# Kernel optimization log

Hardware: AMD Instinct MI355X
Metric: run time of the kernel (lower is better)

Reference implementation:

```python
import jax, jax.numpy as jnp
import numpy as np

N, K, IN, OUT, H = 20000, 32, 128, 256, 64  # H = OUT // 4 (bottleneck hidden)
EPS = 1e-5

def leaky(x):
    return jnp.where(x >= 0, x, 0.1 * x)

def bn(x, g, b, axes):
    # training-mode batch norm: batch statistics over `axes`, per-channel affine
    m = jnp.mean(x, axis=axes, keepdims=True)
    v = jnp.var(x, axis=axes, keepdims=True)
    return (x - m) * jax.lax.rsqrt(v + EPS) * g + b

def setup_inputs() -> dict:
    key = jax.random.key(0)
    ks = jax.random.split(key, 12)
    q_pts = jax.random.normal(ks[0], (N, 3), jnp.float32)
    return {
        'features': jax.random.normal(ks[1], (N, IN), jnp.float32),
        'q_pts': q_pts,
        's_pts': q_pts,  # non-strided block: queries == supports
        'neighb_inds': jax.random.randint(ks[2], (N, K), 0, N, dtype=jnp.int32),
        'w_unary1': jax.random.normal(ks[3], (IN, H), jnp.float32) * 0.05,
        'g1': jnp.ones(H, jnp.float32), 'b1': jnp.zeros(H, jnp.float32),
        'w_conv0': jax.random.normal(ks[4], (H, H), jnp.float32) * 0.05,
        'g_bn0': jnp.ones(H, jnp.float32), 'b_bn0': jnp.zeros(H, jnp.float32),
        'w_conv1': jax.random.normal(ks[5], (H, H * 3), jnp.float32) * 0.05,
        'g_bn1': jnp.ones(H, jnp.float32), 'b_bn1': jnp.zeros(H, jnp.float32),
        'g_bnc': jnp.ones(H, jnp.float32), 'b_bnc': jnp.zeros(H, jnp.float32),
        'w_unary2': jax.random.normal(ks[6], (H, OUT), jnp.float32) * 0.05,
        'g2': jnp.ones(OUT, jnp.float32), 'b2': jnp.zeros(OUT, jnp.float32),
        'w_sc': jax.random.normal(ks[7], (IN, OUT), jnp.float32) * 0.05,
        'g_sc': jnp.ones(OUT, jnp.float32), 'b_sc': jnp.zeros(OUT, jnp.float32),
    }

def reference(features, q_pts, s_pts, neighb_inds,
              w_unary1, g1, b1,
              w_conv0, g_bn0, b_bn0,
              w_conv1, g_bn1, b_bn1,
              g_bnc, b_bnc,
              w_unary2, g2, b2,
              w_sc, g_sc, b_sc):
    # unary1: Linear -> BN1d -> LeakyReLU
    x = leaky(bn(features @ w_unary1, g1, b1, 0))              # [N, H]
    # pad with zero shadow row (index N = out-of-range neighbor)
    s_pad = jnp.concatenate([s_pts, jnp.zeros((1, 3), s_pts.dtype)], 0)
    f_pad = jnp.concatenate([x, jnp.zeros((1, H), x.dtype)], 0)
    nb_x = s_pad[neighb_inds] - q_pts[:, None, :]              # [N, K, 3]
    nb_y = f_pad[neighb_inds]                                  # [N, K, H]
    # adaptive kernel generation: 1x1 conv -> BN2d -> LeakyReLU -> 1x1 conv
    k0 = leaky(bn(jnp.einsum('nkc,cd->nkd', nb_y, w_conv0), g_bn0, b_bn0, (0, 1)))
    kern = jnp.einsum('nkd,de->nke', k0, w_conv1).reshape(N, K, H, 3)
    # per-neighbor dynamic matmul: [H,3] @ [3] per (n,k)
    msg = jnp.einsum('nkhc,nkc->nkh', kern, nb_x)              # [N, K, H]
    msg = leaky(bn(msg, g_bn1, b_bn1, (0, 1)))
    agg = jnp.max(msg, axis=1)                                 # [N, H] max over neighbors
    # batch_norm_conv + LeakyReLU
    agg = leaky(bn(agg, g_bnc, b_bnc, 0))
    # unary2 (no relu) + shortcut (no relu)
    xo = bn(agg @ w_unary2, g2, b2, 0)                         # [N, OUT]
    sc = bn(features @ w_sc, g_sc, b_sc, 0)                    # [N, OUT]
    return leaky(xo + sc)
```

## Files before the change

kernel.cpp:

```cpp
#include <hip/hip_runtime.h>

#define KNB 32
#define CIN 128
#define CH 64
#define COUT 256
#define BN_EPS 1e-5f
#define CONV_GRID 256

typedef __attribute__((ext_vector_type(8))) short bf16x8;
typedef __attribute__((ext_vector_type(4))) float f32x4;

static __device__ __forceinline__ float leakyf(float v){ return fmaxf(v, 0.1f*v); }

static __device__ __forceinline__ unsigned short f2bf(float f){
    unsigned u = __float_as_uint(f);
    u += 0x7FFFu + ((u >> 16) & 1u);
    return (unsigned short)(u >> 16);
}
static __device__ __forceinline__ float bf2f(ushort u){ return __uint_as_float(((unsigned)u) << 16); }

static __device__ __forceinline__ unsigned cvtpk(float lo, float hi){
    unsigned r;
    asm("v_cvt_pk_bf16_f32 %0, %1, %2" : "=v"(r) : "v"(lo), "v"(hi));
    return r;
}

static __device__ __forceinline__ void bn_affine_wave(const float* __restrict__ G, const float* __restrict__ s,
    const float* __restrict__ W, const float* __restrict__ gg, const float* __restrict__ bb,
    float invcnt, int D, int M, int o, int lane, float& ai, float& ci)
{
    float pm = 0.f, pq = 0.f;
    for (int j = lane; j < D; j += 64){
        float wj = W[j*M + o];
        pm += s[j]*wj;
        float t = 0.f;
        for (int i = 0; i < D; ++i) t += G[i*D + j]*W[i*M + o];
        pq += wj*t;
    }
    #pragma unroll
    for (int off = 32; off; off >>= 1){
        pm += __shfl_down(pm, off);
        pq += __shfl_down(pq, off);
    }
    float m  = pm*invcnt;
    float var = pq*invcnt - m*m;
    float a_ = gg[o]*rsqrtf(var + BN_EPS);
    float c_ = bb[o] - m*a_;
    ai = __shfl(a_, 0);
    ci = __shfl(c_, 0);
}

__global__ __launch_bounds__(512) void k1_kernel(const float* __restrict__ feat, const int* __restrict__ inds,
    const float* __restrict__ W1, int N,
    float* __restrict__ slabA, ushort* __restrict__ featbf, ushort* __restrict__ w1s,
    ushort* __restrict__ xbf, float* __restrict__ cnt)
{
    __shared__ ushort Xt[128][40];
    __shared__ float red[16][128];
    int tid = threadIdx.x, bid = blockIdx.x;
    if (bid < 128){
        int wave = tid >> 6, lane = tid & 63, l15 = lane & 15, g = lane >> 4;
        int wr = wave >> 1, wc = wave & 1;
        const f32x4 z4 = {0.f,0.f,0.f,0.f};
        f32x4 acc[2][4];
        #pragma unroll
        for (int i=0;i<2;++i)
            #pragma unroll
            for (int j=0;j<4;++j) acc[i][j] = z4;
        float pcs[4] = {0,0,0,0};
        int nch = (N + 31) >> 5;
        for (int ch = bid; ch < nch; ch += 128){
            int base = ch << 5;
            __syncthreads();
            #pragma unroll
            for (int ii=0; ii<2; ++ii){
                int i = tid + ii*512;
                int r = i >> 5, c4 = i & 31;
                int n = base + r;
                float4 v = make_float4(0.f,0.f,0.f,0.f);
                if (n < N) v = ((const float4*)feat)[(size_t)n*32 + c4];
                ushort b0=f2bf(v.x), b1=f2bf(v.y), b2=f2bf(v.z), b3=f2bf(v.w);
                Xt[c4*4+0][r]=b0; Xt[c4*4+1][r]=b1; Xt[c4*4+2][r]=b2; Xt[c4*4+3][r]=b3;
                pcs[0]+=bf2f(b0); pcs[1]+=bf2f(b1); pcs[2]+=bf2f(b2); pcs[3]+=bf2f(b3);
            }
            __syncthreads();
            bf16x8 af[2], bv[4];
            #pragma unroll
            for (int t=0;t<2;++t) af[t] = *(const bf16x8*)&Xt[wr*32 + t*16 + l15][g*8];
            #pragma unroll
            for (int u=0;u<4;++u) bv[u] = *(const bf16x8*)&Xt[wc*64 + u*16 + l15][g*8];
            #pragma unroll
            for (int t=0;t<2;++t)
                #pragma unroll
                for (int u=0;u<4;++u)
                    acc[t][u] = __builtin_amdgcn_mfma_f32_16x16x32_bf16(af[t], bv[u], acc[t][u], 0,0,0);
        }
        float* Gp = slabA + (size_t)bid*16512;
        #pragma unroll
        for (int t=0;t<2;++t)
            #pragma unroll
            for (int u=0;u<4;++u)
                #pragma unroll
                for (int q=0;q<4;++q)
                    Gp[(wr*32 + t*16 + g*4 + q)*CIN + wc*64 + u*16 + l15] = acc[t][u][q];
        __syncthreads();
        { int r16 = tid >> 5, c4 = tid & 31;
          #pragma unroll
          for (int j=0;j<4;++j) red[r16][c4*4+j] = pcs[j]; }
        __syncthreads();
        if (tid < CIN){
            float s = 0.f;
            #pragma unroll
            for (int k=0;k<16;++k) s += red[k][tid];
            Gp[16384 + tid] = s;
        }
    } else {
        int t2 = (bid-128)*512 + tid;
        const int TG = 128*512;
        for (int i = t2; i < N*32; i += TG){
            float4 v = ((const float4*)feat)[i];
            uint2 pk; pk.x = cvtpk(v.x, v.y); pk.y = cvtpk(v.z, v.w);
            ((uint2*)featbf)[i] = pk;
        }
        for (int i = t2; i < N*KNB; i += TG){
            int ix = inds[i];
            if ((unsigned)ix < (unsigned)N) atomicAdd(&cnt[ix], 1.0f);
        }
        if (t2 < 192*CH){
            int r = t2 >> 6, dd = t2 & 63;
            int c = r >> 6, h = r & 63;
            w1s[t2] = f2bf(W1[dd*192 + 3*h + c]);
        }
        if (t2 < CH) xbf[(size_t)N*CH + t2] = 0;
    }
}

__global__ __launch_bounds__(256) void reduce_slab(const float* __restrict__ slab, int nparts, int len,
                                                   float* __restrict__ dst)
{
    int j = blockIdx.x*256 + threadIdx.x;
    if (j < len){
        float s0 = 0.f, s1 = 0.f, s2 = 0.f, s3 = 0.f;
        int b = 0;
        for (; b + 4 <= nparts; b += 4){
            s0 += slab[(size_t)(b+0)*len + j];
            s1 += slab[(size_t)(b+1)*len + j];
            s2 += slab[(size_t)(b+2)*len + j];
            s3 += slab[(size_t)(b+3)*len + j];
        }
        for (; b < nparts; ++b) s0 += slab[(size_t)b*len + j];
        dst[j] = (s0 + s1) + (s2 + s3);
    }
}

__global__ __launch_bounds__(512) void k3_finA(const float* __restrict__ XtX, const float* __restrict__ fsum,
    const float* __restrict__ Wu1, const float* __restrict__ g1, const float* __restrict__ b1,
    const float* __restrict__ Wsc, const float* __restrict__ gsc, const float* __restrict__ bsc,
    float invN, float* __restrict__ c1v, ushort* __restrict__ w1t,
    ushort* __restrict__ wcat, float* __restrict__ cscv)
{
    int gw = blockIdx.x*8 + (threadIdx.x >> 6), lane = threadIdx.x & 63;
    if (gw < 64){
        int o = gw; float ai, ci;
        bn_affine_wave(XtX, fsum, Wu1, g1, b1, invN, CIN, CH, o, lane, ai, ci);
        if (lane == 0) c1v[o] = ci;
        for (int k = lane; k < CIN; k += 64) w1t[o*CIN + k] = f2bf(ai*Wu1[k*CH + o]);
    } else if (gw < 320){
        int o = gw - 64; float ai, ci;
        bn_affine_wave(XtX, fsum, Wsc, gsc, bsc, invN, CIN, COUT, o, lane, ai, ci);
        if (lane == 0) cscv[o] = ci;
        for (int k = lane; k < CIN; k += 64) wcat[o*192 + k] = f2bf(ai*Wsc[k*COUT + o]);
    }
}

__global__ __launch_bounds__(512) void k4_unary1_gram(const ushort* __restrict__ featbf,
    const ushort* __restrict__ w1t, const float* __restrict__ c1v, const float* __restrict__ cnt,
    ushort* __restrict__ xbf, float* __restrict__ slabB, int N)
{
    __shared__ ushort Xp[64][136];
    __shared__ ushort Xw[64][136];
    __shared__ float red[8][64];
    int tid = threadIdx.x, bid = blockIdx.x;
    int wave = tid >> 6, lane = tid & 63, l15 = lane & 15, g = lane >> 4;
    const f32x4 z4 = {0.f,0.f,0.f,0.f};
    int row0 = bid*128 + wave*16;
    f32x4 acc[4] = {z4, z4, z4, z4};
    int r = row0 + l15;
    bool ok = r < N;
    #pragma unroll
    for (int s=0;s<4;++s){
        bf16x8 af = {0,0,0,0,0,0,0,0};
        if (ok) af = *(const bf16x8*)(featbf + (size_t)r*CIN + s*32 + g*8);
        #pragma unroll
        for (int nt=0;nt<4;++nt){
            bf16x8 bfr = *(const bf16x8*)(w1t + (size_t)(nt*16+l15)*CIN + s*32 + g*8);
            acc[nt] = __builtin_amdgcn_mfma_f32_16x16x32_bf16(af, bfr, acc[nt], 0,0,0);
        }
    }
    float wq[4];
    #pragma unroll
    for (int q=0;q<4;++q){
        int rr = row0 + g*4 + q;
        wq[q] = (rr < N) ? cnt[rr] : 0.f;
    }
    float ps[4] = {0,0,0,0};
    #pragma unroll
    for (int nt=0;nt<4;++nt){
        int col = nt*16 + l15;
        float cc = c1v[col];
        #pragma unroll
        for (int q=0;q<4;++q){
            int rr = row0 + g*4 + q;
            int lr = wave*16 + g*4 + q;
            float v = (rr < N) ? leakyf(acc[nt][q] + cc) : 0.f;
            ushort b = f2bf(v);
            if (rr < N) xbf[(size_t)rr*CH + col] = b;
            Xp[col][lr] = b;
            float wv = wq[q]*v;
            Xw[col][lr] = f2bf(wv);
            ps[nt] += wv;
        }
    }
    #pragma unroll
    for (int nt=0;nt<4;++nt){
        ps[nt] += __shfl_xor(ps[nt], 16);
        ps[nt] += __shfl_xor(ps[nt], 32);
        if (lane < 16) red[wave][nt*16 + l15] = ps[nt];
    }
    __syncthreads();
    int mr = wave >> 1, ncb = (wave & 1)*2;
    f32x4 ac2[2] = {z4, z4};
    #pragma unroll
    for (int ks=0;ks<4;++ks){
        bf16x8 af = *(const bf16x8*)&Xw[mr*16 + l15][ks*32 + g*8];
        #pragma unroll
        for (int u=0;u<2;++u){
            bf16x8 bv = *(const bf16x8*)&Xp[(ncb+u)*16 + l15][ks*32 + g*8];
            ac2[u] = __builtin_amdgcn_mfma_f32_16x16x32_bf16(af, bv, ac2[u], 0,0,0);
        }
    }
    float* Gp = slabB + (size_t)bid*4160;
    #pragma unroll
    for (int u=0;u<2;++u)
        #pragma unroll
        for (int q=0;q<4;++q)
            Gp[(mr*16 + g*4 + q)*CH + (ncb+u)*16 + l15] = ac2[u][q];
    if (tid < CH){
        float s = 0.f;
        #pragma unroll
        for (int w8=0;w8<8;++w8) s += red[w8][tid];
        Gp[4096 + tid] = s;
    }
}

__global__ __launch_bounds__(512) void k5_fin0(const float* __restrict__ G0, const float* __restrict__ s0,
    const float* __restrict__ W0, const float* __restrict__ gb0, const float* __restrict__ bb0,
    float invNK, float* __restrict__ c0p, ushort* __restrict__ w0t)
{
    int gw = blockIdx.x*8 + (threadIdx.x >> 6), lane = threadIdx.x & 63;
    if (gw < 64){
        float ai, ci;
        bn_affine_wave(G0, s0, W0, gb0, bb0, invNK, CH, CH, gw, lane, ai, ci);
        if (lane == 0) c0p[gw] = ci;
        w0t[gw*CH + lane] = f2bf(ai*W0[lane*CH + gw]);
    }
}

__global__ __launch_bounds__(512) void conv_msg_mfma(
    const ushort* __restrict__ xbf, const float* __restrict__ qp, const float* __restrict__ sp,
    const int* __restrict__ inds, const ushort* __restrict__ w0t, const ushort* __restrict__ w1s,
    const float* __restrict__ c0p,
    float* __restrict__ mx, float* __restrict__ mn, float* __restrict__ msgpart, int N)
{
    __shared__ unsigned char SM[24576 + 8*12288];
    int tid = threadIdx.x, bid = blockIdx.x;
    int warp = tid >> 6, lane = tid & 63;
    int l15 = lane & 15, g = lane >> 4;
    for (int ch = tid; ch < 1536; ch += 512){
        int r = ch >> 3, c16 = ch & 7;
        uint4 v = ((const uint4*)w1s)[ch];
        *(uint4*)(SM + r*128 + ((c16*16) ^ ((r&7)<<4))) = v;
    }
    bf16x8 wf[8];
    #pragma unroll
    for (int mt=0;mt<4;++mt)
        #pragma unroll
        for (int s=0;s<2;++s)
            wf[mt*2+s] = *(const bf16x8*)(w0t + (mt*16+l15)*CH + s*32 + g*8);
    float c0r[16];
    #pragma unroll
    for (int mt=0;mt<4;++mt)
        #pragma unroll
        for (int q=0;q<4;++q)
            c0r[mt*4+q] = c0p[mt*16 + g*4 + q];
    unsigned char* k0base = SM + 24576 + warp*12288;
    unsigned swz = (unsigned)((l15 & 7) << 4);
    float ps[4] = {0,0,0,0}, pss[4] = {0,0,0,0};
    const f32x4 z4 = {0.f,0.f,0.f,0.f};
    __syncthreads();

    for (int n = bid*8 + warp; n < N; n += CONV_GRID*8){
        int ix0 = inds[n*KNB + l15];
        int ix1 = inds[n*KNB + 16 + l15];
        if ((unsigned)ix0 > (unsigned)N) ix0 = N;
        if ((unsigned)ix1 > (unsigned)N) ix1 = N;
        float qx = qp[n*3+0], qy = qp[n*3+1], qz = qp[n*3+2];
        float nbv[2][3];
        if (ix0 < N){ nbv[0][0]=sp[ix0*3]-qx; nbv[0][1]=sp[ix0*3+1]-qy; nbv[0][2]=sp[ix0*3+2]-qz; }
        else        { nbv[0][0]=-qx; nbv[0][1]=-qy; nbv[0][2]=-qz; }
        if (ix1 < N){ nbv[1][0]=sp[ix1*3]-qx; nbv[1][1]=sp[ix1*3+1]-qy; nbv[1][2]=sp[ix1*3+2]-qz; }
        else        { nbv[1][0]=-qx; nbv[1][1]=-qy; nbv[1][2]=-qz; }
        bf16x8 xf0a = *(const bf16x8*)(xbf + (size_t)ix0*CH +      g*8);
        bf16x8 xf0b = *(const bf16x8*)(xbf + (size_t)ix0*CH + 32 + g*8);
        bf16x8 xf1a = *(const bf16x8*)(xbf + (size_t)ix1*CH +      g*8);
        bf16x8 xf1b = *(const bf16x8*)(xbf + (size_t)ix1*CH + 32 + g*8);
        f32x4 acc0[8];
        #pragma unroll
        for (int i=0;i<8;++i) acc0[i] = z4;
        #pragma unroll
        for (int mt=0;mt<4;++mt){
            acc0[mt*2+0] = __builtin_amdgcn_mfma_f32_16x16x32_bf16(wf[mt*2+0], xf0a, acc0[mt*2+0], 0,0,0);
            acc0[mt*2+0] = __builtin_amdgcn_mfma_f32_16x16x32_bf16(wf[mt*2+1], xf0b, acc0[mt*2+0], 0,0,0);
            acc0[mt*2+1] = __builtin_amdgcn_mfma_f32_16x16x32_bf16(wf[mt*2+0], xf1a, acc0[mt*2+1], 0,0,0);
            acc0[mt*2+1] = __builtin_amdgcn_mfma_f32_16x16x32_bf16(wf[mt*2+1], xf1b, acc0[mt*2+1], 0,0,0);
        }
        #pragma unroll
        for (int mt=0;mt<4;++mt){
            #pragma unroll
            for (int ntk=0;ntk<2;++ntk){
                f32x4 a = acc0[mt*2+ntk];
                float v0 = leakyf(a[0] + c0r[mt*4+0]);
                float v1 = leakyf(a[1] + c0r[mt*4+1]);
                float v2 = leakyf(a[2] + c0r[mt*4+2]);
                float v3 = leakyf(a[3] + c0r[mt*4+3]);
                #pragma unroll
                for (int c=0;c<3;++c){
                    float w = nbv[ntk][c];
                    uint2 pk;
                    pk.x = cvtpk(v0*w, v1*w);
                    pk.y = cvtpk(v2*w, v3*w);
                    *(uint2*)(k0base + (c*32 + ntk*16 + l15)*128 + ((unsigned)(mt*32 + g*8) ^ swz)) = pk;
                }
            }
        }
        f32x4 acc1[8];
        #pragma unroll
        for (int i=0;i<8;++i) acc1[i] = z4;
        #pragma unroll
        for (int c=0;c<3;++c){
            #pragma unroll
            for (int ks=0;ks<2;++ks){
                unsigned co = ((unsigned)(ks*64 + g*16)) ^ swz;
                bf16x8 a0f = *(const bf16x8*)(k0base + (c*32 +      l15)*128 + co);
                bf16x8 a1f = *(const bf16x8*)(k0base + (c*32 + 16 + l15)*128 + co);
                #pragma unroll
                for (int nt=0;nt<4;++nt){
                    bf16x8 bfr = *(const bf16x8*)(SM + (c*64 + nt*16 + l15)*128 + co);
                    acc1[0*4+nt] = __builtin_amdgcn_mfma_f32_16x16x32_bf16(a0f, bfr, acc1[0*4+nt], 0,0,0);
                    acc1[1*4+nt] = __builtin_amdgcn_mfma_f32_16x16x32_bf16(a1f, bfr, acc1[1*4+nt], 0,0,0);
                }
            }
        }
        #pragma unroll
        for (int nt=0;nt<4;++nt){
            float vmx = -3.4e38f, vmn = 3.4e38f, s = 0.f, ssq = 0.f;
            #pragma unroll
            for (int mtk=0;mtk<2;++mtk){
                f32x4 a = acc1[mtk*4+nt];
                #pragma unroll
                for (int q=0;q<4;++q){
                    float v = a[q];
                    vmx = fmaxf(vmx, v); vmn = fminf(vmn, v);
                    s += v; ssq += v*v;
                }
            }
            vmx = fmaxf(vmx, __shfl_xor(vmx, 16)); vmn = fminf(vmn, __shfl_xor(vmn, 16));
            s  += __shfl_xor(s, 16);               ssq += __shfl_xor(ssq, 16);
            vmx = fmaxf(vmx, __shfl_xor(vmx, 32)); vmn = fminf(vmn, __shfl_xor(vmn, 32));
            s  += __shfl_xor(s, 32);               ssq += __shfl_xor(ssq, 32);
            if (lane < 16){
                mx[(size_t)n*CH + nt*16 + l15] = vmx;
                mn[(size_t)n*CH + nt*16 + l15] = vmn;
                ps[nt] += s; pss[nt] += ssq;
            }
        }
    }
    __syncthreads();
    float* red = (float*)SM;
    if (lane < 16){
        #pragma unroll
        for (int nt=0;nt<4;++nt){
            red[warp*128 + nt*16 + l15]        = ps[nt];
            red[1024 + warp*128 + nt*16 + l15] = pss[nt];
        }
    }
    __syncthreads();
    if (tid < 64){
        float s = 0.f, ssq = 0.f;
        #pragma unroll
        for (int w8=0;w8<8;++w8){ s += red[w8*128 + tid]; ssq += red[1024 + w8*128 + tid]; }
        msgpart[(size_t)bid*128 + tid]      = s;
        msgpart[(size_t)bid*128 + 64 + tid] = ssq;
    }
}

__global__ __launch_bounds__(512) void k7_agg(const float* __restrict__ mxb, const float* __restrict__ mnb,
    const float* __restrict__ msgpart, const float* __restrict__ gb1, const float* __restrict__ bb1,
    float* __restrict__ aggb, float* __restrict__ aggpart, int N)
{
    __shared__ float r1[512], r2[512];
    __shared__ float a1ms[64], c1ms[64];
    int tid = threadIdx.x, bid = blockIdx.x;
    {
        int t = tid & 63, seg = tid >> 6;
        float s = 0.f, ss = 0.f;
        for (int r = seg; r < CONV_GRID; r += 8){ s += msgpart[r*128 + t]; ss += msgpart[r*128 + 64 + t]; }
        r1[tid] = s; r2[tid] = ss;
    }
    __syncthreads();
    if (tid < 64){
        float S = 0.f, SS = 0.f;
        #pragma unroll
        for (int k=0;k<8;++k){ S += r1[tid + 64*k]; SS += r2[tid + 64*k]; }
        float invc = 1.0f/((float)N*KNB);
        float m = S*invc, var = SS*invc - m*m;
        float ai = gb1[tid]*rsqrtf(var + BN_EPS);
        a1ms[tid] = ai; c1ms[tid] = bb1[tid] - m*ai;
    }
    __syncthreads();
    int h = tid & 63;
    float ah = a1ms[h], chh = c1ms[h];
    bool useMax = (ah >= 0.f);
    float ps = 0.f, pss = 0.f;
    for (int i = bid*512 + tid; i < N*CH; i += gridDim.x*512){
        float sel = useMax ? mxb[i] : mnb[i];
        float v = leakyf(ah*sel + chh);
        aggb[i] = v; ps += v; pss += v*v;
    }
    __syncthreads();
    r1[tid] = ps; r2[tid] = pss;
    __syncthreads();
    if (tid < 64){
        float S = 0.f, SS = 0.f;
        #pragma unroll
        for (int k=0;k<8;++k){ S += r1[tid + 64*k]; SS += r2[tid + 64*k]; }
        aggpart[(size_t)bid*128 + tid]      = S;
        aggpart[(size_t)bid*128 + 64 + tid] = SS;
    }
}

__global__ __launch_bounds__(512) void k8_gram64t(const float* __restrict__ aggb, const float* __restrict__ aggpart,
    const float* __restrict__ gbc, const float* __restrict__ bbc,
    ushort* __restrict__ a2b2, float* __restrict__ slabC, int N)
{
    __shared__ ushort Xt[64][72];
    __shared__ float red[32][64];
    __shared__ float abncs[64], cbncs[64];
    int tid = threadIdx.x, bid = blockIdx.x;
    int wave = tid >> 6, lane = tid & 63, l15 = lane & 15, g = lane >> 4;
    const f32x4 z4 = {0.f,0.f,0.f,0.f};
    {
        float* r1 = &red[0][0]; float* r2 = r1 + 512;
        int t = tid & 63, seg = tid >> 6;
        float s = 0.f, ss = 0.f;
        for (int r = seg; r < 256; r += 8){ s += aggpart[r*128 + t]; ss += aggpart[r*128 + 64 + t]; }
        r1[tid] = s; r2[tid] = ss;
        __syncthreads();
        if (tid < 64){
            float S = 0.f, SS = 0.f;
            #pragma unroll
            for (int k=0;k<8;++k){ S += r1[tid + 64*k]; SS += r2[tid + 64*k]; }
            float invc = 1.0f/(float)N;
            float m = S*invc, var = SS*invc - m*m;
            float ai = gbc[tid]*rsqrtf(var + BN_EPS);
            abncs[tid] = ai; cbncs[tid] = bbc[tid] - m*ai;
        }
        __syncthreads();
    }
    int wr = wave >> 1, wc = wave & 1;
    f32x4 acc[2] = {z4, z4};
    float pcs[4] = {0,0,0,0};
    int nch = (N + 63) >> 6;
    for (int ch = bid; ch < nch; ch += 256){
        int base = ch << 6;
        __syncthreads();
        #pragma unroll
        for (int ii=0;ii<2;++ii){
            int i = tid + ii*512;
            int r = i >> 4, cq = i & 15;
            int n = base + r;
            float4 v = make_float4(0.f,0.f,0.f,0.f);
            if (n < N){
                v = ((const float4*)aggb)[(size_t)n*16 + cq];
                v.x = leakyf(abncs[cq*4+0]*v.x + cbncs[cq*4+0]);
                v.y = leakyf(abncs[cq*4+1]*v.y + cbncs[cq*4+1]);
                v.z = leakyf(abncs[cq*4+2]*v.z + cbncs[cq*4+2]);
                v.w = leakyf(abncs[cq*4+3]*v.w + cbncs[cq*4+3]);
            }
            uint2 pk; pk.x = cvtpk(v.x, v.y); pk.y = cvtpk(v.z, v.w);
            if (n < N) ((uint2*)a2b2)[(size_t)n*16 + cq] = pk;
            Xt[cq*4+0][r] = (ushort)(pk.x & 0xffff);
            Xt[cq*4+1][r] = (ushort)(pk.x >> 16);
            Xt[cq*4+2][r] = (ushort)(pk.y & 0xffff);
            Xt[cq*4+3][r] = (ushort)(pk.y >> 16);
            pcs[0] += v.x; pcs[1] += v.y; pcs[2] += v.z; pcs[3] += v.w;
        }
        __syncthreads();
        #pragma unroll
        for (int ks=0;ks<2;++ks){
            bf16x8 af = *(const bf16x8*)&Xt[wr*16 + l15][ks*32 + g*8];
            #pragma unroll
            for (int u=0;u<2;++u){
                bf16x8 bv = *(const bf16x8*)&Xt[wc*32 + u*16 + l15][ks*32 + g*8];
                acc[u] = __builtin_amdgcn_mfma_f32_16x16x32_bf16(af, bv, acc[u], 0,0,0);
            }
        }
    }
    float* Gp = slabC + (size_t)bid*4160;
    #pragma unroll
    for (int u=0;u<2;++u)
        #pragma unroll
        for (int q=0;q<4;++q)
            Gp[(wr*16 + g*4 + q)*CH + wc*32 + u*16 + l15] = acc[u][q];
    __syncthreads();
    { int r = tid >> 4, cq = tid & 15;
      #pragma unroll
      for (int j=0;j<4;++j) red[r][cq*4+j] = pcs[j]; }
    __syncthreads();
    if (tid < CH){
        float s = 0.f;
        #pragma unroll
        for (int k=0;k<32;++k) s += red[k][tid];
        Gp[4096 + tid] = s;
    }
}

__global__ __launch_bounds__(512) void k10_fin2(const float* __restrict__ G2, const float* __restrict__ s2,
    const float* __restrict__ Wu2, const float* __restrict__ g2, const float* __restrict__ b2,
    const float* __restrict__ cscv, float invN, ushort* __restrict__ wcat, float* __restrict__ ccomb)
{
    int gw = blockIdx.x*8 + (threadIdx.x >> 6), lane = threadIdx.x & 63;
    if (gw < 256){
        float ai, ci;
        bn_affine_wave(G2, s2, Wu2, g2, b2, invN, CH, COUT, gw, lane, ai, ci);
        wcat[gw*192 + 128 + lane] = f2bf(ai*Wu2[lane*COUT + gw]);
        if (lane == 0) ccomb[gw] = cscv[gw] + ci;
    }
}

__global__ __launch_bounds__(512) void final_mfma_kernel(
    const ushort* __restrict__ featbf, const ushort* __restrict__ a2b2,
    const ushort* __restrict__ wcat, const float* __restrict__ ccomb,
    float* __restrict__ out, int N)
{
    int tid = threadIdx.x, wave = tid >> 6, lane = tid & 63;
    int l15 = lane & 15, g = lane >> 4;
    int row0 = blockIdx.x*128 + wave*16;
    const f32x4 z4 = {0.f,0.f,0.f,0.f};
    f32x4 acc[16];
    #pragma unroll
    for (int i=0;i<16;++i) acc[i] = z4;
    int r = row0 + l15;
    bool ok = r < N;
    #pragma unroll
    for (int s=0;s<6;++s){
        bf16x8 af = {0,0,0,0,0,0,0,0};
        if (ok){
            const ushort* srcp = (s < 4) ? (featbf + (size_t)r*CIN + s*32 + g*8)
                                         : (a2b2  + (size_t)r*CH + (s-4)*32 + g*8);
            af = *(const bf16x8*)srcp;
        }
        #pragma unroll
        for (int nt=0;nt<16;++nt){
            bf16x8 bfr = *(const bf16x8*)(wcat + (nt*16+l15)*192 + s*32 + g*8);
            acc[nt] = __builtin_amdgcn_mfma_f32_16x16x32_bf16(af, bfr, acc[nt], 0,0,0);
        }
    }
    #pragma unroll
    for (int nt=0;nt<16;++nt){
        float cc = ccomb[nt*16 + l15];
        #pragma unroll
        for (int q=0;q<4;++q){
            int rr = row0 + g*4 + q;
            if (rr < N) out[(size_t)rr*COUT + nt*16 + l15] = leakyf(acc[nt][q] + cc);
        }
    }
}

extern "C" void kernel_launch(void* const* d_in, const int* in_sizes, int n_in,
                              void* d_out, int out_size, void* d_ws, size_t ws_size,
                              hipStream_t stream)
{
    const float* feat = (const float*)d_in[0];
    const float* qp   = (const float*)d_in[1];
    const float* sp   = (const float*)d_in[2];
    const int*   inds = (const int*)d_in[3];
    const float* Wu1  = (const float*)d_in[4];
    const float* g1   = (const float*)d_in[5];
    const float* b1   = (const float*)d_in[6];
    const float* W0   = (const float*)d_in[7];
    const float* gb0  = (const float*)d_in[8];
    const float* bb0  = (const float*)d_in[9];
    const float* W1   = (const float*)d_in[10];
    const float* gb1  = (const float*)d_in[11];
    const float* bb1  = (const float*)d_in[12];
    const float* gbc  = (const float*)d_in[13];
    const float* bbc  = (const float*)d_in[14];
    const float* Wu2  = (const float*)d_in[15];
    const float* g2   = (const float*)d_in[16];
    const float* b2   = (const float*)d_in[17];
    const float* Wsc  = (const float*)d_in[18];
    const float* gsc  = (const float*)d_in[19];
    const float* bsc  = (const float*)d_in[20];

    const int N = in_sizes[0] / CIN;

    float* ws   = (float*)d_ws;
    float* XtX  = ws;
    float* fsum = ws + 16384;
    float* G0   = ws + 16512;
    float* s0   = G0 + 4096;
    float* G2   = ws + 16512 + 4160;
    float* s2   = G2 + 4096;
    float* cnt  = ws + 16512 + 8320;
    float* prm  = cnt + N;
    float* c1v  = prm + 64;
    float* c0p  = prm + 192;
    float* cscv = prm + 768;
    float* msgpart = prm + 1536;
    float* aggpart = msgpart + 256*128;
    float* mxb  = aggpart + 256*128;
    float* mnb  = mxb + (size_t)N*CH;
    float* aggb = mnb + (size_t)N*CH;
    ushort* xbf    = (ushort*)(aggb + (size_t)N*CH);
    ushort* featbf = xbf + (size_t)(N+1)*CH;
    ushort* a2b2   = featbf + (size_t)N*CIN;
    ushort* w1s    = a2b2 + (size_t)N*CH;
    ushort* wcat   = w1s + 192*CH;
    ushort* w1t    = wcat + COUT*192;
    ushort* w0t    = w1t + CH*CIN;
    float*  ccomb  = (float*)(w0t + CH*CH);

    float* slabA = mxb;
    float* slabB = aggb;
    float* slabC = mxb;

    const int nTiles = (N + 127)/128;

    hipMemsetAsync(cnt, 0, (size_t)N*sizeof(float), stream);
    k1_kernel<<<256, 512, 0, stream>>>(feat, inds, W1, N, slabA, featbf, w1s, xbf, cnt);
    reduce_slab<<<(16512 + 255)/256, 256, 0, stream>>>(slabA, 128, 16512, XtX);
    k3_finA<<<40, 512, 0, stream>>>(XtX, fsum, Wu1, g1, b1, Wsc, gsc, bsc, 1.0f/N, c1v, w1t, wcat, cscv);
    k4_unary1_gram<<<nTiles, 512, 0, stream>>>(featbf, w1t, c1v, cnt, xbf, slabB, N);
    reduce_slab<<<(4160 + 255)/256, 256, 0, stream>>>(slabB, nTiles, 4160, G0);
    k5_fin0<<<8, 512, 0, stream>>>(G0, s0, W0, gb0, bb0, 1.0f/((float)N*KNB), c0p, w0t);
    conv_msg_mfma<<<CONV_GRID, 512, 0, stream>>>(xbf, qp, sp, inds, w0t, w1s, c0p, mxb, mnb, msgpart, N);
    k7_agg<<<256, 512, 0, stream>>>(mxb, mnb, msgpart, gb1, bb1, aggb, aggpart, N);
    k8_gram64t<<<256, 512, 0, stream>>>(aggb, aggpart, gbc, bbc, a2b2, slabC, N);
    reduce_slab<<<(4160 + 255)/256, 256, 0, stream>>>(slabC, 256, 4160, G2);
    k10_fin2<<<32, 512, 0, stream>>>(G2, s2, Wu2, g2, b2, cscv, 1.0f/N, wcat, ccomb);
    final_mfma_kernel<<<nTiles, 512, 0, stream>>>(featbf, a2b2, wcat, ccomb, (float*)d_out, N);
}
```

Measured before the change: 234.5 us.

## Split per-node conv into two neighbor halves to halve LDS staging, double grid

The per-node adaptive-kernel conv now processes the 32 neighbors in two 16-neighbor halves. Each half computes its first-layer MFMA, writes the scaled k0 fragment to a per-warp LDS buffer half the previous size, and then runs the second-layer MFMA before the next half reuses that buffer. The smaller LDS footprint and fewer live accumulators are meant to let more blocks reside per CU, and the conv grid is doubled to match. The cost is serialisation between the halves within a warp, a larger partial-statistics buffer, and more blocks to reduce afterwards.

```diff
diff --git a/kernel.cpp b/kernel.cpp
--- a/kernel.cpp
+++ b/kernel.cpp
@@ -5,7 +5,7 @@
 #define CH 64
 #define COUT 256
 #define BN_EPS 1e-5f
-#define CONV_GRID 256
+#define CONV_GRID 512
 
 typedef __attribute__((ext_vector_type(8))) short bf16x8;
 typedef __attribute__((ext_vector_type(4))) float f32x4;
@@ -272,7 +272,7 @@
     const float* __restrict__ c0p,
     float* __restrict__ mx, float* __restrict__ mn, float* __restrict__ msgpart, int N)
 {
-    __shared__ unsigned char SM[24576 + 8*12288];
+    __shared__ unsigned char SM[24576 + 8*6144];
     int tid = threadIdx.x, bid = blockIdx.x;
     int warp = tid >> 6, lane = tid & 63;
     int l15 = lane & 15, g = lane >> 4;
@@ -293,7 +293,7 @@
         #pragma unroll
         for (int q=0;q<4;++q)
             c0r[mt*4+q] = c0p[mt*16 + g*4 + q];
-    unsigned char* k0base = SM + 24576 + warp*12288;
+    unsigned char* k0base = SM + 24576 + warp*6144;
     unsigned swz = (unsigned)((l15 & 7) << 4);
     float ps[4] = {0,0,0,0}, pss[4] = {0,0,0,0};
     const f32x4 z4 = {0.f,0.f,0.f,0.f};
@@ -310,54 +310,48 @@
         else        { nbv[0][0]=-qx; nbv[0][1]=-qy; nbv[0][2]=-qz; }
         if (ix1 < N){ nbv[1][0]=sp[ix1*3]-qx; nbv[1][1]=sp[ix1*3+1]-qy; nbv[1][2]=sp[ix1*3+2]-qz; }
         else        { nbv[1][0]=-qx; nbv[1][1]=-qy; nbv[1][2]=-qz; }
-        bf16x8 xf0a = *(const bf16x8*)(xbf + (size_t)ix0*CH +      g*8);
-        bf16x8 xf0b = *(const bf16x8*)(xbf + (size_t)ix0*CH + 32 + g*8);
-        bf16x8 xf1a = *(const bf16x8*)(xbf + (size_t)ix1*CH +      g*8);
-        bf16x8 xf1b = *(const bf16x8*)(xbf + (size_t)ix1*CH + 32 + g*8);
-        f32x4 acc0[8];
-        #pragma unroll
-        for (int i=0;i<8;++i) acc0[i] = z4;
-        #pragma unroll
-        for (int mt=0;mt<4;++mt){
-            acc0[mt*2+0] = __builtin_amdgcn_mfma_f32_16x16x32_bf16(wf[mt*2+0], xf0a, acc0[mt*2+0], 0,0,0);
-            acc0[mt*2+0] = __builtin_amdgcn_mfma_f32_16x16x32_bf16(wf[mt*2+1], xf0b, acc0[mt*2+0], 0,0,0);
-            acc0[mt*2+1] = __builtin_amdgcn_mfma_f32_16x16x32_bf16(wf[mt*2+0], xf1a, acc0[mt*2+1], 0,0,0);
-            acc0[mt*2+1] = __builtin_amdgcn_mfma_f32_16x16x32_bf16(wf[mt*2+1], xf1b, acc0[mt*2+1], 0,0,0);
-        }
-        #pragma unroll
-        for (int mt=0;mt<4;++mt){
-            #pragma unroll
-            for (int ntk=0;ntk<2;++ntk){
-                f32x4 a = acc0[mt*2+ntk];
-                float v0 = leakyf(a[0] + c0r[mt*4+0]);
-                float v1 = leakyf(a[1] + c0r[mt*4+1]);
-                float v2 = leakyf(a[2] + c0r[mt*4+2]);
-                float v3 = leakyf(a[3] + c0r[mt*4+3]);
+        bf16x8 xf[2][2];
+        xf[0][0] = *(const bf16x8*)(xbf + (size_t)ix0*CH +      g*8);
+        xf[0][1] = *(const bf16x8*)(xbf + (size_t)ix0*CH + 32 + g*8);
+        xf[1][0] = *(const bf16x8*)(xbf + (size_t)ix1*CH +      g*8);
+        xf[1][1] = *(const bf16x8*)(xbf + (size_t)ix1*CH + 32 + g*8);
+        f32x4 acc1[8];
+        #pragma unroll
+        for (int i=0;i<8;++i) acc1[i] = z4;
+        #pragma unroll
+        for (int ntk=0;ntk<2;++ntk){
+            f32x4 acc0[4] = {z4, z4, z4, z4};
+            #pragma unroll
+            for (int mt=0;mt<4;++mt){
+                acc0[mt] = __builtin_amdgcn_mfma_f32_16x16x32_bf16(wf[mt*2+0], xf[ntk][0], acc0[mt], 0,0,0);
+                acc0[mt] = __builtin_amdgcn_mfma_f32_16x16x32_bf16(wf[mt*2+1], xf[ntk][1], acc0[mt], 0,0,0);
+            }
+            #pragma unroll
+            for (int mt=0;mt<4;++mt){
+                float v0 = leakyf(acc0[mt][0] + c0r[mt*4+0]);
+                float v1 = leakyf(acc0[mt][1] + c0r[mt*4+1]);
+                float v2 = leakyf(acc0[mt][2] + c0r[mt*4+2]);
+                float v3 = leakyf(acc0[mt][3] + c0r[mt*4+3]);
                 #pragma unroll
                 for (int c=0;c<3;++c){
                     float w = nbv[ntk][c];
                     uint2 pk;
                     pk.x = cvtpk(v0*w, v1*w);
                     pk.y = cvtpk(v2*w, v3*w);
-                    *(uint2*)(k0base + (c*32 + ntk*16 + l15)*128 + ((unsigned)(mt*32 + g*8) ^ swz)) = pk;
+                    *(uint2*)(k0base + c*2048 + l15*128 + ((unsigned)(mt*32 + g*8) ^ swz)) = pk;
                 }
             }
-        }
-        f32x4 acc1[8];
-        #pragma unroll
-        for (int i=0;i<8;++i) acc1[i] = z4;
-        #pragma unroll
-        for (int c=0;c<3;++c){
-            #pragma unroll
-            for (int ks=0;ks<2;++ks){
-                unsigned co = ((unsigned)(ks*64 + g*16)) ^ swz;
-                bf16x8 a0f = *(const bf16x8*)(k0base + (c*32 +      l15)*128 + co);
-                bf16x8 a1f = *(const bf16x8*)(k0base + (c*32 + 16 + l15)*128 + co);
+            #pragma unroll
+            for (int c=0;c<3;++c){
                 #pragma unroll
-                for (int nt=0;nt<4;++nt){
-                    bf16x8 bfr = *(const bf16x8*)(SM + (c*64 + nt*16 + l15)*128 + co);
-                    acc1[0*4+nt] = __builtin_amdgcn_mfma_f32_16x16x32_bf16(a0f, bfr, acc1[0*4+nt], 0,0,0);
-                    acc1[1*4+nt] = __builtin_amdgcn_mfma_f32_16x16x32_bf16(a1f, bfr, acc1[1*4+nt], 0,0,0);
+                for (int ks=0;ks<2;++ks){
+                    unsigned co = ((unsigned)(ks*64 + g*16)) ^ swz;
+                    bf16x8 af = *(const bf16x8*)(k0base + c*2048 + l15*128 + co);
+                    #pragma unroll
+                    for (int nt=0;nt<4;++nt){
+                        bf16x8 bfr = *(const bf16x8*)(SM + (c*64 + nt*16 + l15)*128 + co);
+                        acc1[ntk*4+nt] = __builtin_amdgcn_mfma_f32_16x16x32_bf16(af, bfr, acc1[ntk*4+nt], 0,0,0);
+                    }
                 }
             }
         }
@@ -628,7 +622,7 @@
     float* c0p  = prm + 192;
     float* cscv = prm + 768;
     float* msgpart = prm + 1536;
-    float* aggpart = msgpart + 256*128;
+    float* aggpart = msgpart + CONV_GRID*128;
     float* mxb  = aggpart + 256*128;
     float* mnb  = mxb + (size_t)N*CH;
     float* aggb = mnb + (size_t)N*CH;
```

Result: slower. 251.9 us (+7.4%).
